# Kernel tuning notes

Hardware: AMD Instinct MI355X
Metric: run time of the kernel (lower is better)

## Reference

```python
import jax, jax.numpy as jnp
import numpy as np

# ---- Cl(3,0) Cayley table: blade order [1, e1, e2, e3, e12, e13, e23, e123] ----
_IDX2BM = [0, 1, 2, 4, 3, 5, 6, 7]
_BM2IDX = {b: i for i, b in enumerate(_IDX2BM)}

def _blade_mul(i, j):
    a, b = _IDX2BM[i], _IDX2BM[j]
    s, aa = 0, a >> 1
    while aa:
        s += bin(aa & b).count('1')
        aa >>= 1
    return _BM2IDX[a ^ b], (-1) ** s

_pairs = [(i, j) + _blade_mul(i, j) for i in range(8) for j in range(8) if i != j]
_pairs = [(i, j, k, s) for (i, j, k, s) in _pairs if k != i and k != j]
SRC_I = np.array([p[0] for p in _pairs])  # (42,)
SRC_J = np.array([p[1] for p in _pairs])
TGT   = np.array([p[2] for p in _pairs])
SIGN  = np.array([p[3] for p in _pairs], dtype=np.float32)

ROPE_THETA = 10000.0


def _rope_tables(T, D, dtype):
    inv_freq = 1.0 / (ROPE_THETA ** (jnp.arange(0, D, 2, dtype=jnp.float32) / D))
    freqs = jnp.arange(T, dtype=jnp.float32)[:, None] * inv_freq[None, :]  # (T, D/2)
    emb = jnp.concatenate([freqs, freqs], axis=-1)  # (T, D)
    return jnp.cos(emb).astype(dtype), jnp.sin(emb).astype(dtype)


def _rotate_half(x):
    x1, x2 = jnp.split(x, 2, axis=-1)
    return jnp.concatenate([-x2, x1], axis=-1)


def setup_inputs() -> dict:
    key = jax.random.key(0)
    k1, k2, k3 = jax.random.split(key, 3)
    B, T, N, D = 2, 2048, 8, 128
    d_model = N * D
    mv = jax.random.normal(k1, (B, T, N, D), dtype=jnp.float32)
    # nn.Linear weights, stored as (in, out) for x @ W; scaled like default init
    W_qkv = jax.random.normal(k2, (d_model, 3 * d_model), dtype=jnp.float32) / np.sqrt(d_model)
    W_o = jax.random.normal(k3, (d_model, d_model), dtype=jnp.float32) / np.sqrt(d_model)
    alpha = jnp.ones((8, 8), dtype=jnp.float32) * 0.01  # cayley_mix_init_scale
    return {"mv": mv, "W_qkv": W_qkv, "W_o": W_o, "alpha": alpha}


def reference(mv, W_qkv, W_o, alpha):
    B, T, N, D = mv.shape
    x_flat = mv.reshape(B, T, N * D)
    qkv = (x_flat @ W_qkv).reshape(B, T, 3, N, D)
    q, k, v = qkv[:, :, 0], qkv[:, :, 1], qkv[:, :, 2]  # (B, T, N, D)

    cos, sin = _rope_tables(T, D, mv.dtype)  # (T, D)
    cos = cos[None, :, None, :]
    sin = sin[None, :, None, :]
    q = q * cos + _rotate_half(q) * sin
    k = k * cos + _rotate_half(k) * sin

    # (B, N, T, D)
    q = q.transpose(0, 2, 1, 3)
    k = k.transpose(0, 2, 1, 3)
    v = v.transpose(0, 2, 1, 3)

    scale = 1.0 / jnp.sqrt(jnp.asarray(D, dtype=mv.dtype))
    scores = jnp.einsum('bntd,bnsd->bnts', q, k) * scale  # (B, N, T, T)
    causal = jnp.tril(jnp.ones((T, T), dtype=bool))
    scores = jnp.where(causal[None, None], scores, -jnp.inf)
    attn = jax.nn.softmax(scores, axis=-1)
    out = jnp.einsum('bnts,bnsd->bntd', attn, v)  # (B, N, T, D)

    out = out.transpose(0, 2, 1, 3).reshape(B, T, N * D)
    out = (out @ W_o).reshape(B, T, N, D)

    # Cayley cross-blade mixing
    si, sj, tgt = jnp.asarray(SRC_I), jnp.asarray(SRC_J), jnp.asarray(TGT)
    pair_w = alpha[si, sj] * jnp.asarray(SIGN)  # (42,)
    contrib = out[:, :, si, :] * out[:, :, sj, :] * pair_w[None, None, :, None]
    mixed = jnp.zeros_like(out).at[:, :, tgt, :].add(contrib)
    return out + mixed
```

## Files before the change

kernel.cpp:

```cpp
#include <hip/hip_runtime.h>
#include <stdint.h>


typedef __attribute__((ext_vector_type(8)))  __bf16 bf16x8;
typedef __attribute__((ext_vector_type(4)))  float  f32x4;

__device__ __forceinline__ uint16_t f2bf(float f) {
    uint32_t u = __float_as_uint(f);
    u += 0x7FFFu + ((u >> 16) & 1u);
    return (uint16_t)(u >> 16);
}
__device__ __forceinline__ float bf2f(uint16_t h) {
    return __uint_as_float(((uint32_t)h) << 16);
}

__device__ __forceinline__ void gload_lds16(const void* g, void* l) {
    __builtin_amdgcn_global_load_lds(
        (__attribute__((address_space(1))) void*)g,
        (__attribute__((address_space(3))) void*)l, 16, 0, 0);
}

__global__ __launch_bounds__(256) void k_cast(const float* __restrict__ in,
                                              uint16_t* __restrict__ out, int n) {
    int i = blockIdx.x * 256 + threadIdx.x;
    if (i * 4 >= n) return;
    float4 v = ((const float4*)in)[i];
    ushort4 o = make_ushort4(f2bf(v.x), f2bf(v.y), f2bf(v.z), f2bf(v.w));
    ((ushort4*)out)[i] = o;
}

__global__ __launch_bounds__(256) void k_wtrans(const float* __restrict__ W,
                                                uint16_t* __restrict__ Wt,
                                                int K, int N) {
    __shared__ uint16_t tile[64][65];
    const int k0 = blockIdx.y * 64, n0 = blockIdx.x * 64;
    const int c = threadIdx.x & 63, r4 = threadIdx.x >> 6;
#pragma unroll
    for (int i = 0; i < 16; ++i) {
        int r = r4 + i * 4;
        tile[r][c] = f2bf(W[(size_t)(k0 + r) * N + n0 + c]);
    }
    __syncthreads();
#pragma unroll
    for (int i = 0; i < 16; ++i) {
        int r = r4 + i * 4;
        Wt[(size_t)(n0 + r) * K + k0 + c] = tile[c][r];
    }
}

__global__ __launch_bounds__(256) void k_tab(float* __restrict__ ct,
                                             float* __restrict__ st) {
    int i = blockIdx.x * 256 + threadIdx.x;
    int t = i >> 6, f = i & 63;
    float inv = expf(-(float)f * 0.14391156830441f);
    float ang = (float)t * inv;
    ct[i] = cosf(ang);
    st[i] = sinf(ang);
}

__global__ __launch_bounds__(256) void k_gemmqkv(const uint16_t* __restrict__ A,
                                                 const uint16_t* __restrict__ Bt,
                                                 const float* __restrict__ ct,
                                                 const float* __restrict__ st,
                                                 uint16_t* __restrict__ Qr,
                                                 uint16_t* __restrict__ Kr,
                                                 uint16_t* __restrict__ Vt) {
    __shared__ uint16_t Atile[128 * 32];
    __shared__ uint16_t Btile[128 * 32];
    __shared__ uint16_t Tl[128][132];
    const int bx = blockIdx.x;
    const int m0 = blockIdx.y << 7, n0 = bx << 7;
    const int sec = bx >> 3, head = bx & 7;
    const int tid = threadIdx.x;
    const int l = tid & 63, w = tid >> 6;
    const int lr = l & 15, lg = l >> 4;
    const int wm = (w >> 1) << 6, wn = (w & 1) << 6;
    const int K = 1024;

    f32x4 acc[4][4];
#pragma unroll
    for (int i = 0; i < 4; ++i)
#pragma unroll
        for (int j = 0; j < 4; ++j) acc[i][j] = (f32x4){0.f, 0.f, 0.f, 0.f};

    for (int kt = 0; kt < 32; ++kt) {
        const int k0 = kt << 5;
        __syncthreads();
#pragma unroll
        for (int c = 0; c < 4; ++c) {
            int idx = c * 256 + tid;
            if (idx < 512) {
                int r = idx >> 2, kc = (idx & 3) << 3;
                gload_lds16(A + (size_t)(m0 + r) * K + k0 + kc, &Atile[idx * 8]);
            } else {
                int i2 = idx - 512;
                int r = i2 >> 2, kc = (i2 & 3) << 3;
                gload_lds16(Bt + (size_t)(n0 + r) * K + k0 + kc, &Btile[i2 * 8]);
            }
        }
        __syncthreads();
        bf16x8 af[4], bfv[4];
#pragma unroll
        for (int i = 0; i < 4; ++i) {
            af[i]  = *(const bf16x8*)(&Atile[(wm + i * 16 + lr) * 32 + lg * 8]);
            bfv[i] = *(const bf16x8*)(&Btile[(wn + i * 16 + lr) * 32 + lg * 8]);
        }
#pragma unroll
        for (int mi = 0; mi < 4; ++mi)
#pragma unroll
            for (int ni = 0; ni < 4; ++ni)
                acc[mi][ni] = __builtin_amdgcn_mfma_f32_16x16x32_bf16(
                    af[mi], bfv[ni], acc[mi][ni], 0, 0, 0);
    }

    __syncthreads();
#pragma unroll
    for (int mi = 0; mi < 4; ++mi)
#pragma unroll
        for (int ni = 0; ni < 4; ++ni)
#pragma unroll
            for (int r = 0; r < 4; ++r)
                Tl[wm + mi * 16 + lg * 4 + r][wn + ni * 16 + lr] =
                    f2bf(acc[mi][ni][r]);
    __syncthreads();

    const int b = m0 >> 11, t0 = m0 & 2047;
    const size_t hidx = (size_t)(b * 8 + head);
    if (sec < 2) {
        uint16_t* outp = (sec == 0 ? Qr : Kr) + (hidx * 2048 + t0) * 128;
#pragma unroll
        for (int it = 0; it < 8; ++it) {
            int lin = it * 256 + tid;
            int tr = lin >> 4, d0 = (lin & 15) * 4;
            ushort4 lo = *(const ushort4*)&Tl[tr][d0];
            ushort4 hi = *(const ushort4*)&Tl[tr][d0 + 64];
            float4 cv = *(const float4*)&ct[(size_t)(t0 + tr) * 64 + d0];
            float4 sv = *(const float4*)&st[(size_t)(t0 + tr) * 64 + d0];
            ushort4 o1, o2;
            o1.x = f2bf(bf2f(lo.x) * cv.x - bf2f(hi.x) * sv.x);
            o2.x = f2bf(bf2f(hi.x) * cv.x + bf2f(lo.x) * sv.x);
            o1.y = f2bf(bf2f(lo.y) * cv.y - bf2f(hi.y) * sv.y);
            o2.y = f2bf(bf2f(hi.y) * cv.y + bf2f(lo.y) * sv.y);
            o1.z = f2bf(bf2f(lo.z) * cv.z - bf2f(hi.z) * sv.z);
            o2.z = f2bf(bf2f(hi.z) * cv.z + bf2f(lo.z) * sv.z);
            o1.w = f2bf(bf2f(lo.w) * cv.w - bf2f(hi.w) * sv.w);
            o2.w = f2bf(bf2f(hi.w) * cv.w + bf2f(lo.w) * sv.w);
            *(ushort4*)&outp[(size_t)tr * 128 + d0]      = o1;
            *(ushort4*)&outp[(size_t)tr * 128 + d0 + 64] = o2;
        }
    } else {
        uint16_t* vp = Vt + hidx * 128 * 2048;
#pragma unroll
        for (int it = 0; it < 8; ++it) {
            int lin = it * 256 + tid;
            int d = lin >> 4, tq = (lin & 15) * 8;
            ushort4 v0 = make_ushort4(Tl[tq + 0][d], Tl[tq + 1][d],
                                      Tl[tq + 2][d], Tl[tq + 3][d]);
            ushort4 v1 = make_ushort4(Tl[tq + 4][d], Tl[tq + 5][d],
                                      Tl[tq + 6][d], Tl[tq + 7][d]);
            *(ushort4*)&vp[(size_t)d * 2048 + t0 + tq]     = v0;
            *(ushort4*)&vp[(size_t)d * 2048 + t0 + tq + 4] = v1;
        }
    }
}

__global__ __launch_bounds__(256) void k_gemm2s(const uint16_t* __restrict__ A,
                                                const uint16_t* __restrict__ Bt,
                                                float* __restrict__ C) {
    __shared__ uint16_t Atile[128 * 32];
    __shared__ uint16_t Btile[128 * 32];
    const int kz = blockIdx.z;
    A  += (size_t)kz * 512;
    Bt += (size_t)kz * 512;
    C  += (size_t)kz * (4096u * 1024u);
    const int m0 = blockIdx.y << 7, n0 = blockIdx.x << 7;
    const int tid = threadIdx.x;
    const int l = tid & 63, w = tid >> 6;
    const int lr = l & 15, lg = l >> 4;
    const int wm = (w >> 1) << 6, wn = (w & 1) << 6;

    f32x4 acc[4][4];
#pragma unroll
    for (int i = 0; i < 4; ++i)
#pragma unroll
        for (int j = 0; j < 4; ++j) acc[i][j] = (f32x4){0.f, 0.f, 0.f, 0.f};

    for (int kt = 0; kt < 16; ++kt) {
        const int k0 = kt << 5;
        __syncthreads();
#pragma unroll
        for (int c = 0; c < 4; ++c) {
            int idx = c * 256 + tid;
            if (idx < 512) {
                int r = idx >> 2, kc = (idx & 3) << 3;
                gload_lds16(A + (size_t)(m0 + r) * 1024 + k0 + kc, &Atile[idx * 8]);
            } else {
                int i2 = idx - 512;
                int r = i2 >> 2, kc = (i2 & 3) << 3;
                gload_lds16(Bt + (size_t)(n0 + r) * 1024 + k0 + kc, &Btile[i2 * 8]);
            }
        }
        __syncthreads();
        bf16x8 af[4], bfv[4];
#pragma unroll
        for (int i = 0; i < 4; ++i) {
            af[i]  = *(const bf16x8*)(&Atile[(wm + i * 16 + lr) * 32 + lg * 8]);
            bfv[i] = *(const bf16x8*)(&Btile[(wn + i * 16 + lr) * 32 + lg * 8]);
        }
#pragma unroll
        for (int mi = 0; mi < 4; ++mi)
#pragma unroll
            for (int ni = 0; ni < 4; ++ni)
                acc[mi][ni] = __builtin_amdgcn_mfma_f32_16x16x32_bf16(
                    af[mi], bfv[ni], acc[mi][ni], 0, 0, 0);
    }
#pragma unroll
    for (int mi = 0; mi < 4; ++mi)
#pragma unroll
        for (int ni = 0; ni < 4; ++ni)
#pragma unroll
            for (int r = 0; r < 4; ++r) {
                int row = m0 + wm + mi * 16 + lg * 4 + r;
                int col = n0 + wn + ni * 16 + lr;
                C[(size_t)row * 1024 + col] = acc[mi][ni][r];
            }
}

__global__ __launch_bounds__(256) void k_attn(const uint16_t* __restrict__ Qg,
                                              const uint16_t* __restrict__ Kg,
                                              const uint16_t* __restrict__ Vtg,
                                              uint16_t* __restrict__ AOg) {
    __shared__ uint16_t Klds[2][64 * 128];
    __shared__ uint16_t Vlds[2][128 * 64];
    __shared__ uint16_t Plds[4][16 * 64];

    const int bx = blockIdx.x;
    const int h  = bx & 15;
    const int t4 = (bx >> 4) & 15;
    const int qt = (bx < 256) ? (31 - t4) : t4;
    const int q0 = qt * 64;
    const int tid = threadIdx.x;
    const int l = tid & 63, w = tid >> 6;
    const int lr = l & 15, lg = l >> 4;
    const size_t headTD = (size_t)h * (2048 * 128);
    const uint16_t* Kh = Kg + headTD;
    const uint16_t* Vh = Vtg + headTD;

    bf16x8 qf[4];
    {
        const uint16_t* qp = Qg + headTD + (size_t)(q0 + w * 16 + lr) * 128 + lg * 8;
#pragma unroll
        for (int kc = 0; kc < 4; ++kc) qf[kc] = *(const bf16x8*)(qp + kc * 32);
    }

    f32x4 accO[8];
#pragma unroll
    for (int i = 0; i < 8; ++i) accO[i] = (f32x4){0.f, 0.f, 0.f, 0.f};
    float mrun = -1e30f, lrun = 0.f;

    const float SL2E = 0.08838834764831845f * 1.4426950408889634f;
    const int   swz  = (lr & 7) << 4;
    uint16_t* Pw = &Plds[w][0];

    auto STAGE = [&](int buf, int k0) {
#pragma unroll
        for (int p = 0; p < 4; ++p) {
            int u = p * 256 + tid;
            int row = u >> 4;
            int c16 = (u & 15) ^ (row & 7);
            gload_lds16(Kh + (size_t)(k0 + row) * 128 + c16 * 8,
                        (char*)&Klds[buf][0] + u * 16);
        }
#pragma unroll
        for (int p = 0; p < 4; ++p) {
            int u = p * 256 + tid;
            int d = u >> 3;
            int c8 = (u & 7) ^ (d & 7);
            gload_lds16(Vh + (size_t)d * 2048 + k0 + c8 * 8,
                        (char*)&Vlds[buf][0] + u * 16);
        }
    };

    STAGE(0, 0);

    for (int kt = 0; kt <= qt; ++kt) {
        asm volatile("s_waitcnt vmcnt(0)" ::: "memory");
        __builtin_amdgcn_s_barrier();
        __builtin_amdgcn_sched_barrier(0);
        if (kt < qt) STAGE((kt + 1) & 1, (kt + 1) * 64);

        const char* Kb = (const char*)&Klds[kt & 1][0];
        const char* Vb = (const char*)&Vlds[kt & 1][0];

        float sv[4][4];
        __builtin_amdgcn_s_setprio(1);
#pragma unroll
        for (int cg = 0; cg < 4; ++cg) {
            f32x4 a = (f32x4){0.f, 0.f, 0.f, 0.f};
#pragma unroll
            for (int kc = 0; kc < 4; ++kc) {
                int kb = (cg * 16 + lr) * 256 + ((kc * 64 + lg * 16) ^ swz);
                bf16x8 kf = *(const bf16x8*)(Kb + kb);
                a = __builtin_amdgcn_mfma_f32_16x16x32_bf16(kf, qf[kc], a, 0, 0, 0);
            }
#pragma unroll
            for (int r = 0; r < 4; ++r) sv[cg][r] = a[r];
        }
        __builtin_amdgcn_s_setprio(0);

        if (kt == qt) {
#pragma unroll
            for (int cg = 0; cg < 4; ++cg)
#pragma unroll
                for (int r = 0; r < 4; ++r)
                    if (cg * 16 + lg * 4 + r > w * 16 + lr) sv[cg][r] = -1e30f;
        }

        float pml = sv[0][0];
#pragma unroll
        for (int cg = 0; cg < 4; ++cg)
#pragma unroll
            for (int r = 0; r < 4; ++r) pml = fmaxf(pml, sv[cg][r]);

        if (!__all(pml * SL2E <= mrun + 11.f)) {
            float mx = pml;
            mx = fmaxf(mx, __shfl_xor(mx, 16, 64));
            mx = fmaxf(mx, __shfl_xor(mx, 32, 64));
            float mn = fmaxf(mrun, mx * SL2E);
            float corr = exp2f(mrun - mn);
            mrun = mn;
            lrun *= corr;
            float ca[4];
#pragma unroll
            for (int r = 0; r < 4; ++r)
                ca[r] = __shfl(corr, (lg << 4) + lg * 4 + r, 64);
#pragma unroll
            for (int i = 0; i < 8; ++i)
#pragma unroll
                for (int r = 0; r < 4; ++r) accO[i][r] *= ca[r];
        }

        float psum = 0.f;
        float p[4][4];
#pragma unroll
        for (int cg = 0; cg < 4; ++cg)
#pragma unroll
            for (int r = 0; r < 4; ++r) {
                p[cg][r] = exp2f(fmaf(sv[cg][r], SL2E, -mrun));
                psum += p[cg][r];
            }
        lrun += psum;

#pragma unroll
        for (int cg = 0; cg < 4; ++cg) {
            uint32_t w0, w1;
            asm("v_cvt_pk_bf16_f32 %0, %1, %2" : "=v"(w0) : "v"(p[cg][0]), "v"(p[cg][1]));
            asm("v_cvt_pk_bf16_f32 %0, %1, %2" : "=v"(w1) : "v"(p[cg][2]), "v"(p[cg][3]));
            uint2 pr; pr.x = w0; pr.y = w1;
            *(uint2*)((char*)Pw + lr * 128 + ((cg * 32 + lg * 8) ^ swz)) = pr;
        }

        asm volatile("" ::: "memory");
        bf16x8 pf[2];
#pragma unroll
        for (int c = 0; c < 2; ++c)
            pf[c] = *(const bf16x8*)((char*)Pw + lr * 128 + ((c * 64 + lg * 16) ^ swz));

        __builtin_amdgcn_s_setprio(1);
#pragma unroll
        for (int ni = 0; ni < 8; ++ni)
#pragma unroll
            for (int c = 0; c < 2; ++c) {
                int vb = (ni * 16 + lr) * 128 + ((c * 64 + lg * 16) ^ swz);
                bf16x8 vf = *(const bf16x8*)(Vb + vb);
                accO[ni] = __builtin_amdgcn_mfma_f32_16x16x32_bf16(pf[c], vf, accO[ni], 0, 0, 0);
            }
        __builtin_amdgcn_s_setprio(0);
    }

    float lsum = lrun;
    lsum += __shfl_xor(lsum, 16, 64);
    lsum += __shfl_xor(lsum, 32, 64);
    float linv = 1.f / lsum;
    float inv[4];
#pragma unroll
    for (int r = 0; r < 4; ++r)
        inv[r] = __shfl(linv, (lg << 4) + lg * 4 + r, 64);
    const int b = h >> 3, n = h & 7;
#pragma unroll
    for (int ni = 0; ni < 8; ++ni)
#pragma unroll
        for (int r = 0; r < 4; ++r) {
            int trow = q0 + w * 16 + lg * 4 + r;
            AOg[((size_t)(b * 2048 + trow)) * 1024 + n * 128 + ni * 16 + lr] =
                f2bf(accO[ni][r] * inv[r]);
        }
}

__global__ __launch_bounds__(256) void k_mix(const float* __restrict__ out0,
                                             const float* __restrict__ out1,
                                             const float* __restrict__ alpha,
                                             float* __restrict__ fin) {
    constexpr int SI[42] = {1,1,1,1,1,1, 2,2,2,2,2,2, 3,3,3,3,3,3, 4,4,4,4,4,4,
                            5,5,5,5,5,5, 6,6,6,6,6,6, 7,7,7,7,7,7};
    constexpr int SJ[42] = {2,3,4,5,6,7, 1,3,4,5,6,7, 1,2,4,5,6,7, 1,2,3,5,6,7,
                            1,2,3,4,6,7, 1,2,3,4,5,7, 1,2,3,4,5,6};
    constexpr int TG[42] = {4,5,2,3,7,6, 4,6,1,7,3,5, 5,6,7,1,2,4, 2,1,7,6,5,3,
                            3,7,1,6,4,2, 7,3,2,5,4,1, 6,5,4,3,2,1};
    constexpr float SG[42] = {+1,+1,+1,+1,+1,+1, -1,+1,-1,-1,+1,-1, -1,-1,+1,-1,-1,+1,
                              -1,+1,+1,-1,+1,-1, -1,-1,+1,+1,-1,+1, +1,-1,+1,-1,+1,-1,
                              +1,-1,+1,-1,+1,-1};
    int idx = blockIdx.x * 256 + threadIdx.x;
    int d = idx & 127, bt = idx >> 7;
    size_t base = (size_t)bt * 1024 + d;
    float o[8], r[8];
#pragma unroll
    for (int hh = 0; hh < 8; ++hh) {
        o[hh] = out0[base + hh * 128] + out1[base + hh * 128];
        r[hh] = o[hh];
    }
#pragma unroll
    for (int p = 0; p < 42; ++p)
        r[TG[p]] += alpha[SI[p] * 8 + SJ[p]] * SG[p] * o[SI[p]] * o[SJ[p]];
#pragma unroll
    for (int hh = 0; hh < 8; ++hh) fin[base + hh * 128] = r[hh];
}

extern "C" void kernel_launch(void* const* d_in, const int* in_sizes, int n_in,
                              void* d_out, int out_size, void* d_ws, size_t ws_size,
                              hipStream_t stream) {
    (void)in_sizes; (void)n_in; (void)out_size; (void)ws_size;
    const float* mv    = (const float*)d_in[0];
    const float* Wqkv  = (const float*)d_in[1];
    const float* Wo    = (const float*)d_in[2];
    const float* alpha = (const float*)d_in[3];
    float* outp = (float*)d_out;
    char* ws = (char*)d_ws;

    uint16_t* Xbf  = (uint16_t*)(ws + 0);
    uint16_t* Wqt  = (uint16_t*)(ws + 8388608);
    uint16_t* Wot  = (uint16_t*)(ws + 14680064);
    uint16_t* Qr   = (uint16_t*)(ws + 41943040);
    uint16_t* Kr   = (uint16_t*)(ws + 50331648);
    uint16_t* Vt   = (uint16_t*)(ws + 58720256);
    float*    ctab = (float*)(ws + 67108864);
    float*    stab = (float*)(ws + 67633152);
    uint16_t* AO   = (uint16_t*)(ws + 0);
    float*    outF0 = (float*)(ws + 16777216);
    float*    outF1 = (float*)(ws + 33554432);

    k_cast   <<<4096, 256, 0, stream>>>(mv, Xbf, 4096 * 1024);
    k_wtrans <<<dim3(48, 16), 256, 0, stream>>>(Wqkv, Wqt, 1024, 3072);
    k_wtrans <<<dim3(16, 16), 256, 0, stream>>>(Wo, Wot, 1024, 1024);
    k_tab    <<<512, 256, 0, stream>>>(ctab, stab);
    k_gemmqkv<<<dim3(24, 32), 256, 0, stream>>>(Xbf, Wqt, ctab, stab, Qr, Kr, Vt);
    k_attn   <<<512, 256, 0, stream>>>(Qr, Kr, Vt, AO);
    k_gemm2s <<<dim3(8, 32, 2), 256, 0, stream>>>(AO, Wot, outF0);
    k_mix    <<<2048, 256, 0, stream>>>(outF0, outF1, alpha, outp);
}
```

Before: 137.0 us.

## Remap GEMM blocks across XCDs, shrink out-proj tile, vectorize Cayley mix

The QKV GEMM and the output-projection GEMM now remap linear block IDs so that consecutive hardware blocks, which are dispatched round-robin over the 8 XCDs, land on neighbouring logical tiles on the same XCD. This is meant to improve L2 reuse. The output-projection GEMM moves to 128x64 tiles, doubling the grid to raise occupancy and wave count on a small problem, at the cost of more A-tile reloads. The mix kernel now processes four contiguous d values per thread with float4 loads and stores, cutting the thread count and index overhead.

```diff
diff --git a/kernel.cpp b/kernel.cpp
--- a/kernel.cpp
+++ b/kernel.cpp
@@ -68,8 +68,10 @@
     __shared__ uint16_t Atile[128 * 32];
     __shared__ uint16_t Btile[128 * 32];
     __shared__ uint16_t Tl[128][132];
-    const int bx = blockIdx.x;
-    const int m0 = blockIdx.y << 7, n0 = bx << 7;
+    const int lin = blockIdx.y * 24 + blockIdx.x;
+    const int logical = (lin & 7) * 96 + (lin >> 3);
+    const int bx = logical % 24;
+    const int m0 = (logical / 24) << 7, n0 = bx << 7;
     const int sec = bx >> 3, head = bx & 7;
     const int tid = threadIdx.x;
     const int l = tid & 63, w = tid >> 6;
@@ -130,8 +132,8 @@
         uint16_t* outp = (sec == 0 ? Qr : Kr) + (hidx * 2048 + t0) * 128;
 #pragma unroll
         for (int it = 0; it < 8; ++it) {
-            int lin = it * 256 + tid;
-            int tr = lin >> 4, d0 = (lin & 15) * 4;
+            int lin2 = it * 256 + tid;
+            int tr = lin2 >> 4, d0 = (lin2 & 15) * 4;
             ushort4 lo = *(const ushort4*)&Tl[tr][d0];
             ushort4 hi = *(const ushort4*)&Tl[tr][d0 + 64];
             float4 cv = *(const float4*)&ct[(size_t)(t0 + tr) * 64 + d0];
@@ -152,8 +154,8 @@
         uint16_t* vp = Vt + hidx * 128 * 2048;
 #pragma unroll
         for (int it = 0; it < 8; ++it) {
-            int lin = it * 256 + tid;
-            int d = lin >> 4, tq = (lin & 15) * 8;
+            int lin2 = it * 256 + tid;
+            int d = lin2 >> 4, tq = (lin2 & 15) * 8;
             ushort4 v0 = make_ushort4(Tl[tq + 0][d], Tl[tq + 1][d],
                                       Tl[tq + 2][d], Tl[tq + 3][d]);
             ushort4 v1 = make_ushort4(Tl[tq + 4][d], Tl[tq + 5][d],
@@ -168,28 +170,30 @@
                                                 const uint16_t* __restrict__ Bt,
                                                 float* __restrict__ C) {
     __shared__ uint16_t Atile[128 * 32];
-    __shared__ uint16_t Btile[128 * 32];
+    __shared__ uint16_t Btile[64 * 32];
     const int kz = blockIdx.z;
     A  += (size_t)kz * 512;
     Bt += (size_t)kz * 512;
     C  += (size_t)kz * (4096u * 1024u);
-    const int m0 = blockIdx.y << 7, n0 = blockIdx.x << 7;
+    const int lin = blockIdx.y * 16 + blockIdx.x;
+    const int logical = (lin & 7) * 64 + (lin >> 3);
+    const int m0 = (logical >> 4) << 7, n0 = (logical & 15) << 6;
     const int tid = threadIdx.x;
     const int l = tid & 63, w = tid >> 6;
     const int lr = l & 15, lg = l >> 4;
-    const int wm = (w >> 1) << 6, wn = (w & 1) << 6;
-
-    f32x4 acc[4][4];
+    const int wm = (w >> 1) << 6, wn = (w & 1) << 5;
+
+    f32x4 acc[4][2];
 #pragma unroll
     for (int i = 0; i < 4; ++i)
 #pragma unroll
-        for (int j = 0; j < 4; ++j) acc[i][j] = (f32x4){0.f, 0.f, 0.f, 0.f};
+        for (int j = 0; j < 2; ++j) acc[i][j] = (f32x4){0.f, 0.f, 0.f, 0.f};
 
     for (int kt = 0; kt < 16; ++kt) {
         const int k0 = kt << 5;
         __syncthreads();
 #pragma unroll
-        for (int c = 0; c < 4; ++c) {
+        for (int c = 0; c < 3; ++c) {
             int idx = c * 256 + tid;
             if (idx < 512) {
                 int r = idx >> 2, kc = (idx & 3) << 3;
@@ -201,23 +205,24 @@
             }
         }
         __syncthreads();
-        bf16x8 af[4], bfv[4];
-#pragma unroll
-        for (int i = 0; i < 4; ++i) {
-            af[i]  = *(const bf16x8*)(&Atile[(wm + i * 16 + lr) * 32 + lg * 8]);
-            bfv[i] = *(const bf16x8*)(&Btile[(wn + i * 16 + lr) * 32 + lg * 8]);
-        }
+        bf16x8 af[4], bfv[2];
+#pragma unroll
+        for (int i = 0; i < 4; ++i)
+            af[i] = *(const bf16x8*)(&Atile[(wm + i * 16 + lr) * 32 + lg * 8]);
+#pragma unroll
+        for (int j = 0; j < 2; ++j)
+            bfv[j] = *(const bf16x8*)(&Btile[(wn + j * 16 + lr) * 32 + lg * 8]);
 #pragma unroll
         for (int mi = 0; mi < 4; ++mi)
 #pragma unroll
-            for (int ni = 0; ni < 4; ++ni)
+            for (int ni = 0; ni < 2; ++ni)
                 acc[mi][ni] = __builtin_amdgcn_mfma_f32_16x16x32_bf16(
                     af[mi], bfv[ni], acc[mi][ni], 0, 0, 0);
     }
 #pragma unroll
     for (int mi = 0; mi < 4; ++mi)
 #pragma unroll
-        for (int ni = 0; ni < 4; ++ni)
+        for (int ni = 0; ni < 2; ++ni)
 #pragma unroll
             for (int r = 0; r < 4; ++r) {
                 int row = m0 + wm + mi * 16 + lg * 4 + r;
@@ -411,19 +416,26 @@
                               -1,+1,+1,-1,+1,-1, -1,-1,+1,+1,-1,+1, +1,-1,+1,-1,+1,-1,
                               +1,-1,+1,-1,+1,-1};
     int idx = blockIdx.x * 256 + threadIdx.x;
-    int d = idx & 127, bt = idx >> 7;
-    size_t base = (size_t)bt * 1024 + d;
-    float o[8], r[8];
+    int dq = (idx & 31) * 4, bt = idx >> 5;
+    size_t base = (size_t)bt * 1024 + dq;
+    float4 o[8], r[8];
 #pragma unroll
     for (int hh = 0; hh < 8; ++hh) {
-        o[hh] = out0[base + hh * 128] + out1[base + hh * 128];
+        float4 a = *(const float4*)&out0[base + hh * 128];
+        float4 b = *(const float4*)&out1[base + hh * 128];
+        o[hh] = make_float4(a.x + b.x, a.y + b.y, a.z + b.z, a.w + b.w);
         r[hh] = o[hh];
     }
 #pragma unroll
-    for (int p = 0; p < 42; ++p)
-        r[TG[p]] += alpha[SI[p] * 8 + SJ[p]] * SG[p] * o[SI[p]] * o[SJ[p]];
-#pragma unroll
-    for (int hh = 0; hh < 8; ++hh) fin[base + hh * 128] = r[hh];
+    for (int p = 0; p < 42; ++p) {
+        float wgt = alpha[SI[p] * 8 + SJ[p]] * SG[p];
+        r[TG[p]].x += wgt * o[SI[p]].x * o[SJ[p]].x;
+        r[TG[p]].y += wgt * o[SI[p]].y * o[SJ[p]].y;
+        r[TG[p]].z += wgt * o[SI[p]].z * o[SJ[p]].z;
+        r[TG[p]].w += wgt * o[SI[p]].w * o[SJ[p]].w;
+    }
+#pragma unroll
+    for (int hh = 0; hh < 8; ++hh) *(float4*)&fin[base + hh * 128] = r[hh];
 }
 
 extern "C" void kernel_launch(void* const* d_in, const int* in_sizes, int n_in,
@@ -455,6 +467,6 @@
     k_tab    <<<512, 256, 0, stream>>>(ctab, stab);
     k_gemmqkv<<<dim3(24, 32), 256, 0, stream>>>(Xbf, Wqt, ctab, stab, Qr, Kr, Vt);
     k_attn   <<<512, 256, 0, stream>>>(Qr, Kr, Vt, AO);
-    k_gemm2s <<<dim3(8, 32, 2), 256, 0, stream>>>(AO, Wot, outF0);
-    k_mix    <<<2048, 256, 0, stream>>>(outF0, outF1, alpha, outp);
-}
+    k_gemm2s <<<dim3(16, 32, 2), 256, 0, stream>>>(AO, Wot, outF0);
+    k_mix    <<<512, 256, 0, stream>>>(outF0, outF1, alpha, outp);
+}
```

After: 133.9 us. 1.02x faster.
